# Kernel tuning notes

Measured on AMD Instinct MI355X. Metric: run time of the kernel, lower is better.

## Reference

```python
import jax, jax.numpy as jnp
import numpy as np

N_NODES = 50000
N_EDGES = 800000
GEN_EPS = 1e-7
LN_EPS = 1e-5


def _mlp3_tanh(x, w0, b0, w1, b1, w2, b2):
    x = jnp.tanh(x @ w0.T + b0)
    x = jnp.tanh(x @ w1.T + b1)
    return jnp.tanh(x @ w2.T + b2)


def _gen_conv(x, src, dst, edge_attr, w0, b0, ln_w, ln_b, w1, b1):
    # GENConv(aggr='softmax', t=1): msg = relu(x_j + e) + eps
    msg = jax.nn.relu(x[src] + edge_attr) + GEN_EPS          # [E, 64]
    m = jax.ops.segment_max(msg, dst, num_segments=N_NODES)  # [N, 64]
    ex = jnp.exp(msg - m[dst])
    den = jax.ops.segment_sum(ex, dst, num_segments=N_NODES)
    alpha = ex / den[dst]                                    # scatter-softmax per dst
    agg = jax.ops.segment_sum(alpha * msg, dst, num_segments=N_NODES)
    h = x + agg                                              # x_r + aggregated messages
    # internal MLP: Linear(64->128), LayerNorm(128), ReLU, Linear(128->64)
    h = h @ w0.T + b0
    mu = jnp.mean(h, axis=-1, keepdims=True)
    var = jnp.mean((h - mu) ** 2, axis=-1, keepdims=True)
    h = ln_w * (h - mu) * jax.lax.rsqrt(var + LN_EPS) + ln_b
    h = jax.nn.relu(h)
    return h @ w1.T + b1


def setup_inputs() -> dict:
    key = jax.random.key(0)
    ks = jax.random.split(key, 32)
    s = 0.05
    d = {
        'node_features': jax.random.normal(ks[0], (N_NODES, 11), jnp.float32),
        'edge_features': jax.random.normal(ks[1], (N_EDGES, 3), jnp.float32),
        'edge_index': jax.random.randint(ks[2], (2, N_EDGES), 0, N_NODES, jnp.int32),
        'ne_w0': jax.random.normal(ks[3], (64, 11)) * s, 'ne_b0': jnp.zeros((64,)),
        'ne_w1': jax.random.normal(ks[4], (64, 64)) * s, 'ne_b1': jnp.zeros((64,)),
        'ne_w2': jax.random.normal(ks[5], (64, 64)) * s, 'ne_b2': jnp.zeros((64,)),
        'ee_w0': jax.random.normal(ks[6], (64, 3)) * s, 'ee_b0': jnp.zeros((64,)),
        'ee_w1': jax.random.normal(ks[7], (64, 64)) * s, 'ee_b1': jnp.zeros((64,)),
        'ee_w2': jax.random.normal(ks[8], (64, 64)) * s, 'ee_b2': jnp.zeros((64,)),
        'mp_w0': jax.random.normal(ks[9], (3, 128, 64)) * s,
        'mp_b0': jnp.zeros((3, 128)),
        'mp_ln_w': jnp.ones((3, 128)), 'mp_ln_b': jnp.zeros((3, 128)),
        'mp_w1': jax.random.normal(ks[10], (3, 64, 128)) * s,
        'mp_b1': jnp.zeros((3, 64)),
        'pi_w0': jax.random.normal(ks[11], (64, 64)) * s, 'pi_b0': jnp.zeros((64,)),
        'pi_w1': jax.random.normal(ks[12], (64, 64)) * s, 'pi_b1': jnp.zeros((64,)),
        'pi_w2': jax.random.normal(ks[13], (2, 64)) * s, 'pi_b2': jnp.zeros((2,)),
    }
    return {k: (v.astype(jnp.float32) if v.dtype != jnp.int32 else v) for k, v in d.items()}


def reference(node_features, edge_features, edge_index,
              ne_w0, ne_b0, ne_w1, ne_b1, ne_w2, ne_b2,
              ee_w0, ee_b0, ee_w1, ee_b1, ee_w2, ee_b2,
              mp_w0, mp_b0, mp_ln_w, mp_ln_b, mp_w1, mp_b1,
              pi_w0, pi_b0, pi_w1, pi_b1, pi_w2, pi_b2):
    src, dst = edge_index[0], edge_index[1]
    x = _mlp3_tanh(node_features, ne_w0, ne_b0, ne_w1, ne_b1, ne_w2, ne_b2)
    e = _mlp3_tanh(edge_features, ee_w0, ee_b0, ee_w1, ee_b1, ee_w2, ee_b2)
    for i in range(3):
        x = _gen_conv(x, src, dst, e, mp_w0[i], mp_b0[i], mp_ln_w[i], mp_ln_b[i], mp_w1[i], mp_b1[i])
    h = jnp.tanh(x @ pi_w0.T + pi_b0)
    h = jnp.tanh(h @ pi_w1.T + pi_b1)
    out = h @ pi_w2.T + pi_b2                 # [N, 2]
    # output.t().reshape(-1)[:n_turbines] == first column of out
    means = -30.0 + (out[:, 0] + 1.0) * 60.0 / 2.0
    return means
```

## Files before the change

kernel.cpp:

```cpp
#include <hip/hip_runtime.h>
#include <stdint.h>

#define N_NODES 50000
#define N_EDGES 800000

typedef unsigned short u16;
typedef unsigned int u32;
typedef __attribute__((ext_vector_type(8))) short short8;
typedef __attribute__((ext_vector_type(4))) float f32x4;
typedef __attribute__((ext_vector_type(4))) u32 u32x4;
typedef __attribute__((ext_vector_type(2))) u32 u32x2;

#define WAVE_SYNC() asm volatile("s_waitcnt lgkmcnt(0)" ::: "memory")

__device__ __forceinline__ float b2f(u16 v) {
    u32 u = ((u32)v) << 16; float f; __builtin_memcpy(&f, &u, 4); return f;
}
__device__ __forceinline__ u16 f2b(float f) {
    u32 u; __builtin_memcpy(&u, &f, 4);
    return (u16)((u + 0x8000u) >> 16);
}
__device__ __forceinline__ float lo2f(u32 p) {
    u32 u = p << 16; float f; __builtin_memcpy(&f, &u, 4); return f;
}
__device__ __forceinline__ float hi2f(u32 p) {
    u32 u = p & 0xffff0000u; float f; __builtin_memcpy(&f, &u, 4); return f;
}
__device__ __forceinline__ u32 pack2(float a, float b) {
    u32 ua, ub; __builtin_memcpy(&ua, &a, 4); __builtin_memcpy(&ub, &b, 4);
    return __builtin_amdgcn_perm(ub + 0x8000u, ua + 0x8000u, 0x07060302u);
}
__device__ __forceinline__ f32x4 mfma16(short8 a, short8 b, f32x4 c) {
    return __builtin_amdgcn_mfma_f32_16x16x32_bf16(a, b, c, 0, 0, 0);
}

#define TANH_TBL_N 192
__device__ __forceinline__ void load_tbl(const float2* __restrict__ g, float2* tbl) {
    int i = (int)threadIdx.x;
    if (i < TANH_TBL_N) tbl[i] = g[i];
    __syncthreads();
}
__device__ __forceinline__ float lut_tanh(const float2* __restrict__ tbl, float x) {
    float a = __builtin_fabsf(x);
    a = fminf(a, 5.96875f);
    int i = (int)(a * 32.f);
    float2 bs = tbl[i];
    float y = fmaf(bs.y, a, bs.x);
    return copysignf(y, x);
}

enum : int {
    NE_T0 = 0,     NE_B0 = 704,   NE_T1 = 768,   NE_B1 = 4864,  NE_T2 = 4928,  NE_B2 = 9024,
    EE_T0 = 9088,  EE_B0 = 9280,  EE_T1 = 9344,  EE_B1 = 13440, EE_T2 = 13504, EE_B2 = 17600,
    MP_T0 = 17664, MP_B0 = 42240, LNW_O = 42624, LNB_O = 43008, MP_T1 = 43392, MP_B1 = 67968,
    PI_T0 = 68160, PI_B0 = 72256, PI_T1 = 72320, PI_B1 = 76416, PI_W2 = 76480, PI_B2 = 76608,
    W_TOTAL = 76610
};

enum : int {
    FR_EE1 = 0, FR_EE2 = 4, FR_EE3 = 12, FR_NE1 = 20, FR_NE2 = 24, FR_NE3 = 32,
    FR_MP0 = 40, FR_MP1 = 88, FR_PI0 = 136, FR_PI1 = 144, FR_TOTAL = 152
};

#define OFF_W       ((size_t)0)
#define OFF_FLAG    ((size_t)0x60000)
#define OFF_WB      ((size_t)0x61000)
#define OFF_TBL     ((size_t)0x88000)
#define OFF_XB0     ((size_t)0x90000)
#define OFF_XB1     ((size_t)0x700000)
#define OFF_H64B    ((size_t)0xE00000)
#define OFF_E       ((size_t)0x1500000)
#define OFF_ROWPTR  ((size_t)0x8300000)
#define OFF_CURSOR  ((size_t)0x8340000)
#define OFF_CNT     ((size_t)0x8380000)
#define OFF_PERM    ((size_t)0x83C0000)
#define OFF_SRCS    ((size_t)0x8700000)
#define OFF_BSUM    ((size_t)0x8A80000)

struct Ptrs24 { const void* p[24]; };


__global__ void detect_kernel(const void* nf, int* flag) {
    u32 w = ((const u32*)nf)[threadIdx.x & 63];
    u32 lo = w & 0xffffu;
    int e = (int)((lo >> 7) & 0xff);
    int good = ((e >= 118 && e <= 132) || lo == 0) ? 1 : 0;
    unsigned long long b = __ballot(good != 0);
    if (threadIdx.x == 0) *flag = (__popcll(b) >= 48) ? 1 : 0;
}

__global__ void convert_weights(Ptrs24 ps, float* __restrict__ W, const int* flag) {
    const int segIN[24] = {11,64,64,64,64,64, 3,64,64,64,64,64, 64,384,384,384,128,192, 64,64,64,64,128,2};
    const int segOUT[24]= {64, 1,64, 1,64, 1, 64, 1,64, 1,64, 1, 128, 1,  1,  1, 64,  1, 64, 1,64, 1,  1,1};
    const int segS[24]  = { 1, 1, 1, 1, 1, 1,  1, 1, 1, 1, 1, 1,   3, 1,  1,  1,  3,  1,  1, 1, 1, 1,  1,1};
    const int segTR[24] = { 1, 0, 1, 0, 1, 0,  1, 0, 1, 0, 1, 0,   1, 0,  0,  0,  1,  0,  1, 0, 1, 0,  0,0};
    int t = blockIdx.x * blockDim.x + threadIdx.x;
    if (t >= W_TOTAL) return;
    bool bf = (*flag != 0);
    int seg = 0, off = t;
    for (;;) {
        int cnt = segIN[seg] * segOUT[seg] * segS[seg];
        if (off < cnt) break;
        off -= cnt; seg++;
    }
    int srcIdx;
    if (segTR[seg]) {
        int per = segIN[seg] * segOUT[seg];
        int s = off / per, d = off % per;
        int j = d / segOUT[seg], i = d % segOUT[seg];
        srcIdx = s * per + i * segIN[seg] + j;
    } else {
        srcIdx = off;
    }
    const void* p = ps.p[seg];
    W[t] = bf ? b2f(((const u16*)p)[srcIdx]) : ((const float*)p)[srcIdx];
}

__global__ void make_frags(const float* __restrict__ W, u16* __restrict__ Wb,
                           float2* __restrict__ gtbl) {
    const int base[15] = {FR_EE1,FR_EE2,FR_EE3,FR_NE1,FR_NE2,FR_NE3,
                          FR_MP0,FR_MP0+16,FR_MP0+32, FR_MP1,FR_MP1+16,FR_MP1+32,
                          FR_PI0,FR_PI1,FR_TOTAL};
    const int woff[14] = {EE_T0,EE_T1,EE_T2, NE_T0,NE_T1,NE_T2,
                          MP_T0,MP_T0+8192,MP_T0+16384, MP_T1,MP_T1+8192,MP_T1+16384,
                          PI_T0,PI_T1};
    const int kreal[14] = {3,64,64, 11,64,64, 64,64,64, 128,128,128, 64,64};
    const int nn[14]    = {64,64,64, 64,64,64, 128,128,128, 64,64,64, 64,64};
    int t = blockIdx.x * blockDim.x + threadIdx.x;
    if (t >= FR_TOTAL * 512) {
        int i = t - FR_TOTAL * 512;
        if (i < TANH_TBL_N) {
            float x0 = i * 0.03125f, x1 = x0 + 0.03125f;
            float t0 = tanhf(x0), t1 = tanhf(x1);
            float s = (t1 - t0) * 32.f;
            gtbl[i] = make_float2(fmaf(-s, x0, t0), s);
        }
        return;
    }
    int f = t >> 9, r = t & 511, lane = r >> 3, j = r & 7;
    int l = 0;
    while (f >= base[l + 1]) l++;
    int lf = f - base[l];
    int NT = nn[l] >> 4;
    int kt = lf / NT, nt = lf % NT;
    int k = kt * 32 + (lane >> 4) * 8 + j;
    int n = nt * 16 + (lane & 15);
    float v = (k < kreal[l]) ? W[woff[l] + k * nn[l] + n] : 0.f;
    u32 u; __builtin_memcpy(&u, &v, 4);
    Wb[t] = (u16)((u + 0x7fffu + ((u >> 16) & 1u)) >> 16);
}


__global__ void hist_kernel(const int* __restrict__ dst, int* __restrict__ cnts) {
    int e = blockIdx.x * blockDim.x + threadIdx.x;
    if (e < N_EDGES) atomicAdd(&cnts[dst[e]], 1);
}

__global__ void scanA(const int* __restrict__ cnts, int* __restrict__ prow,
                      int* __restrict__ bsum) {
    __shared__ int wsum[16];
    int tid = threadIdx.x, lane = tid & 63, wid = tid >> 6;
    int i0 = blockIdx.x * 2048 + tid * 2;
    int v0 = 0, v1 = 0;
    if (i0 >= 1 && i0 <= N_NODES) v0 = (cnts[i0 - 1] + 1) & ~1;
    if (i0 + 1 <= N_NODES && i0 + 1 >= 1) v1 = (cnts[i0] + 1) & ~1;
    int v = v0 + v1;
#pragma unroll
    for (int off = 1; off < 64; off <<= 1) {
        int t = __shfl_up(v, off, 64);
        if (lane >= off) v += t;
    }
    if (lane == 63) wsum[wid] = v;
    __syncthreads();
    if (tid == 0) { int a = 0; for (int w = 0; w < 16; w++) { a += wsum[w]; wsum[w] = a; } }
    __syncthreads();
    int incl = v + (wid ? wsum[wid - 1] : 0);
    if (i0 <= N_NODES) prow[i0] = incl - v1;
    if (i0 + 1 <= N_NODES) prow[i0 + 1] = incl;
    if (tid == 1023) bsum[blockIdx.x] = incl;
}
__global__ void scanC(const int* __restrict__ bsum, int* __restrict__ prow,
                      int* __restrict__ cursor) {
    int i = blockIdx.x * 1024 + threadIdx.x;
    if (i > N_NODES) return;
    int nb = (int)(blockIdx.x >> 1);
    int add = 0;
    for (int b = 0; b < nb; b++) add += bsum[b];
    int v = prow[i] + add;
    prow[i] = v;
    if (i < N_NODES) cursor[i] = v;
}

__global__ void scatter_kernel(const int* __restrict__ dst, const int* __restrict__ src,
                               int* __restrict__ cursor, int* __restrict__ perm,
                               int* __restrict__ srcs) {
    int e = blockIdx.x * blockDim.x + threadIdx.x;
    if (e >= N_EDGES) return;
    int p = atomicAdd(&cursor[dst[e]], 1);
    perm[e] = p;
    srcs[p] = src[e];
}


template<int KT, int NT, int INSTR>
__device__ __forceinline__ void mfma_layer(const u32* ldsin, int lane,
        const short8* __restrict__ Wf, int basef, const float* __restrict__ bias, f32x4* acc) {
    int q = lane >> 4, mr = lane & 15;
#pragma unroll
    for (int nt = 0; nt < NT; nt++) acc[nt] = *(const f32x4*)(bias + nt * 16 + q * 4);
#pragma unroll
    for (int kt = 0; kt < KT; kt++) {
        short8 act = *(const short8*)(ldsin + mr * INSTR + kt * 16 + q * 4);
#pragma unroll
        for (int nt = 0; nt < NT; nt++)
            acc[nt] = mfma16(Wf[(basef + kt * NT + nt) * 64 + lane], act, acc[nt]);
    }
}

template<int KT, int NT>
__device__ __forceinline__ void mfma_layer_reg(const short8* act, int lane,
        const short8* __restrict__ Wf, int basef, const float* __restrict__ bias, f32x4* acc) {
    int q = lane >> 4;
#pragma unroll
    for (int nt = 0; nt < NT; nt++) acc[nt] = *(const f32x4*)(bias + nt * 16 + q * 4);
#pragma unroll
    for (int kt = 0; kt < KT; kt++)
#pragma unroll
        for (int nt = 0; nt < NT; nt++)
            acc[nt] = mfma16(Wf[(basef + kt * NT + nt) * 64 + lane], act[kt], acc[nt]);
}

template<int NT, int OUTSTR>
__device__ __forceinline__ void tanh_pack_lds(const f32x4* acc, u32* ldsout, int lane,
                                              const float2* __restrict__ tbl) {
    int q = lane >> 4, mr = lane & 15;
#pragma unroll
    for (int nt = 0; nt < NT; nt++) {
        f32x4 a = acc[nt];
        ldsout[mr * OUTSTR + nt * 8 + q * 2 + 0] = pack2(lut_tanh(tbl, a[0]), lut_tanh(tbl, a[1]));
        ldsout[mr * OUTSTR + nt * 8 + q * 2 + 1] = pack2(lut_tanh(tbl, a[2]), lut_tanh(tbl, a[3]));
    }
}

__device__ __forceinline__ void zero_stage(u32* B0, int lane) {
#pragma unroll
    for (int it = 0; it < 4; it++) {
        int f = lane + 64 * it;
        B0[(f >> 4) * 36 + (f & 15)] = 0;
    }
}


__global__ __launch_bounds__(256) void edge_encoder(const void* ef, u32* __restrict__ ebuf,
        const int* __restrict__ perm, const float* __restrict__ W,
        const short8* __restrict__ Wf, const float2* __restrict__ gtbl, const int* flag) {
    __shared__ u32 lds[4 * 1152];
    __shared__ float2 tbl[TANH_TBL_N];
    load_tbl(gtbl, tbl);
    int wv = threadIdx.x >> 6, lane = threadIdx.x & 63;
    u32* B0 = lds + wv * 1152;
    u32* B1 = B0 + 576;
    long ebase = (long)blockIdx.x * 64 + wv * 16;
    bool bf = (*flag != 0);
    zero_stage(B0, lane);
    if (lane < 16) {
        long e = ebase + lane;
        float i0, i1, i2;
        if (bf) { const u16* p = (const u16*)ef + e * 3; i0 = b2f(p[0]); i1 = b2f(p[1]); i2 = b2f(p[2]); }
        else    { const float* p = (const float*)ef + e * 3; i0 = p[0]; i1 = p[1]; i2 = p[2]; }
        u32* row = B0 + lane * 36;
        row[0] = pack2(i0, i1); row[1] = pack2(i2, 0.f);
    }
    WAVE_SYNC();
    f32x4 acc[4];
    mfma_layer<1, 4, 36>(B0, lane, Wf, FR_EE1, W + EE_B0, acc);
    tanh_pack_lds<4, 36>(acc, B1, lane, tbl);
    WAVE_SYNC();
    mfma_layer<2, 4, 36>(B1, lane, Wf, FR_EE2, W + EE_B1, acc);
    tanh_pack_lds<4, 36>(acc, B0, lane, tbl);
    WAVE_SYNC();
    mfma_layer<2, 4, 36>(B0, lane, Wf, FR_EE3, W + EE_B2, acc);
    tanh_pack_lds<4, 36>(acc, B1, lane, tbl);
    WAVE_SYNC();
    int ro = lane >> 2, cc = (lane & 3) * 8;
    long e = ebase + ro;
    long prowp = perm[e];
    u32x4 v0 = *(const u32x4*)&B1[ro * 36 + cc];
    u32x4 v1 = *(const u32x4*)&B1[ro * 36 + cc + 4];
    *(u32x4*)&ebuf[prowp * 32 + cc] = v0;
    *(u32x4*)&ebuf[prowp * 32 + cc + 4] = v1;
}

__global__ __launch_bounds__(256) void node_encoder(const void* nf,
        u16* __restrict__ xbf, const float* __restrict__ W,
        const short8* __restrict__ Wf, const float2* __restrict__ gtbl, const int* flag) {
    __shared__ u32 lds[4 * 1152];
    __shared__ float2 tbl[TANH_TBL_N];
    load_tbl(gtbl, tbl);
    int wv = threadIdx.x >> 6, lane = threadIdx.x & 63;
    int q = lane >> 4, mr = lane & 15;
    u32* B0 = lds + wv * 1152;
    u32* B1 = B0 + 576;
    long nbase = (long)blockIdx.x * 64 + wv * 16;
    bool bf = (*flag != 0);
    zero_stage(B0, lane);
    if (lane < 16) {
        long n = nbase + lane;
        if (n < N_NODES) {
            float in[11];
#pragma unroll
            for (int j = 0; j < 11; j++)
                in[j] = bf ? b2f(((const u16*)nf)[n * 11 + j]) : ((const float*)nf)[n * 11 + j];
            u32* row = B0 + lane * 36;
#pragma unroll
            for (int d = 0; d < 5; d++) row[d] = pack2(in[2 * d], in[2 * d + 1]);
            row[5] = pack2(in[10], 0.f);
        }
    }
    WAVE_SYNC();
    f32x4 acc[4];
    mfma_layer<1, 4, 36>(B0, lane, Wf, FR_NE1, W + NE_B0, acc);
    tanh_pack_lds<4, 36>(acc, B1, lane, tbl);
    WAVE_SYNC();
    mfma_layer<2, 4, 36>(B1, lane, Wf, FR_NE2, W + NE_B1, acc);
    tanh_pack_lds<4, 36>(acc, B0, lane, tbl);
    WAVE_SYNC();
    mfma_layer<2, 4, 36>(B0, lane, Wf, FR_NE3, W + NE_B2, acc);
    long n = nbase + mr;
    if (n < N_NODES) {
#pragma unroll
        for (int nt = 0; nt < 4; nt++) {
            float v0 = lut_tanh(tbl, acc[nt][0]), v1 = lut_tanh(tbl, acc[nt][1]);
            float v2 = lut_tanh(tbl, acc[nt][2]), v3 = lut_tanh(tbl, acc[nt][3]);
            u32x2 pb; pb.x = pack2(v0, v1); pb.y = pack2(v2, v3);
            *(u32x2*)&xbf[n * 64 + nt * 16 + q * 4] = pb;
        }
    }
}

__global__ __launch_bounds__(256) void aggregate_kernel(
        const u32* __restrict__ xbf32, const u32* __restrict__ ebuf32,
        const int* __restrict__ srcs, const int* __restrict__ prow,
        u32* __restrict__ h64bf32) {
    __shared__ int ldsW[4][64];
    int wv = threadIdx.x >> 6;
    int wid = (int)((blockIdx.x * 256 + threadIdx.x) >> 6);
    int lane = (int)(threadIdx.x & 63);
    int n0 = __builtin_amdgcn_readfirstlane(wid) * 2;
    if (n0 >= N_NODES) return;
    int half = lane >> 5, h = lane & 31;
    int rl = n0 + (lane < 2 ? lane : 2);
    int rv = prow[rl];
    int kb0 = __shfl(rv, 0, 64);
    int kb1 = __shfl(rv, 1, 64);
    int kb2 = __shfl(rv, 2, 64);
    float num[2][2], den[2][2];
#pragma unroll
    for (int j = 0; j < 2; j++) { num[j][0] = num[j][1] = den[j][0] = den[j][1] = 0.f; }
    for (int wb = kb0; wb < kb2; wb += 64) {
        ldsW[wv][lane] = srcs[wb + lane];
        WAVE_SYNC();
        int we = wb + 64;
        int hi0 = kb1 < we ? kb1 : we;
        int lo1 = kb1 > wb ? kb1 : wb;
        int hi1 = kb2 < we ? kb2 : we;
#pragma unroll 2
        for (int k = wb; k < hi0; k += 2) {
            int s = ldsW[wv][k - wb + half];
            u32 ev = ebuf32[(size_t)(k + half) * 32 + h];
            u32 xv = xbf32[(size_t)(s > 0 ? s : 0) * 32 + h];
            float m0 = fmaxf(lo2f(xv) + lo2f(ev), 0.f) + 1e-7f;
            float m1 = fmaxf(hi2f(xv) + hi2f(ev), 0.f) + 1e-7f;
            float w0 = __expf(m0), w1 = __expf(m1);
            if (s < 0) { w0 = 0.f; w1 = 0.f; }
            num[0][0] = fmaf(w0, m0, num[0][0]); den[0][0] += w0;
            num[0][1] = fmaf(w1, m1, num[0][1]); den[0][1] += w1;
        }
#pragma unroll 2
        for (int k = lo1; k < hi1; k += 2) {
            int s = ldsW[wv][k - wb + half];
            u32 ev = ebuf32[(size_t)(k + half) * 32 + h];
            u32 xv = xbf32[(size_t)(s > 0 ? s : 0) * 32 + h];
            float m0 = fmaxf(lo2f(xv) + lo2f(ev), 0.f) + 1e-7f;
            float m1 = fmaxf(hi2f(xv) + hi2f(ev), 0.f) + 1e-7f;
            float w0 = __expf(m0), w1 = __expf(m1);
            if (s < 0) { w0 = 0.f; w1 = 0.f; }
            num[1][0] = fmaf(w0, m0, num[1][0]); den[1][0] += w0;
            num[1][1] = fmaf(w1, m1, num[1][1]); den[1][1] += w1;
        }
        WAVE_SYNC();
    }
#pragma unroll
    for (int j = 0; j < 2; j++) {
        float n0f = num[j][0] + __shfl_xor(num[j][0], 32, 64);
        float d0f = den[j][0] + __shfl_xor(den[j][0], 32, 64);
        float n1f = num[j][1] + __shfl_xor(num[j][1], 32, 64);
        float d1f = den[j][1] + __shfl_xor(den[j][1], 32, 64);
        if (half == 0) {
            float agg0 = (d0f > 0.f) ? __fdividef(n0f, d0f) : 0.f;
            float agg1 = (d1f > 0.f) ? __fdividef(n1f, d1f) : 0.f;
            u32 xr = xbf32[(size_t)(n0 + j) * 32 + h];
            h64bf32[(size_t)(n0 + j) * 32 + h] = pack2(lo2f(xr) + agg0, hi2f(xr) + agg1);
        }
    }
}

__global__ __launch_bounds__(256) void mlp_fused(const u16* __restrict__ h64bf,
        u16* __restrict__ xbf,
        const float* __restrict__ W, const short8* __restrict__ Wf, int r) {
    __shared__ u32 lds[4 * 1088];
    int wv = threadIdx.x >> 6, lane = threadIdx.x & 63;
    int q = lane >> 4, mr = lane & 15;
    u32* bufY = lds + wv * 1088;
    long nbase = (long)blockIdx.x * 64 + wv * 16;
    long row = nbase + mr;
    long rc = (row < N_NODES) ? row : (N_NODES - 1);
    short8 act[2];
#pragma unroll
    for (int kt = 0; kt < 2; kt++)
        act[kt] = *(const short8*)&h64bf[rc * 64 + kt * 32 + q * 8];
    f32x4 acc[8];
    mfma_layer_reg<2, 8>(act, lane, Wf, FR_MP0 + r * 16, W + MP_B0 + r * 128, acc);
    float s = 0.f, sq = 0.f;
#pragma unroll
    for (int nt = 0; nt < 8; nt++)
#pragma unroll
        for (int rr = 0; rr < 4; rr++) { float v = acc[nt][rr]; s += v; sq = fmaf(v, v, sq); }
    s += __shfl_xor(s, 16, 64);  s += __shfl_xor(s, 32, 64);
    sq += __shfl_xor(sq, 16, 64); sq += __shfl_xor(sq, 32, 64);
    float mu = s * (1.f / 128.f);
    float var = sq * (1.f / 128.f) - mu * mu;
    float inv = rsqrtf(var + 1e-5f);
    const float* LW = W + LNW_O + r * 128;
    const float* LB = W + LNB_O + r * 128;
#pragma unroll
    for (int nt = 0; nt < 8; nt++) {
        f32x4 lw = *(const f32x4*)(LW + nt * 16 + q * 4);
        f32x4 lb = *(const f32x4*)(LB + nt * 16 + q * 4);
        float u0 = fmaxf(fmaf((acc[nt][0] - mu) * inv, lw[0], lb[0]), 0.f);
        float u1 = fmaxf(fmaf((acc[nt][1] - mu) * inv, lw[1], lb[1]), 0.f);
        float u2 = fmaxf(fmaf((acc[nt][2] - mu) * inv, lw[2], lb[2]), 0.f);
        float u3 = fmaxf(fmaf((acc[nt][3] - mu) * inv, lw[3], lb[3]), 0.f);
        bufY[mr * 68 + nt * 8 + q * 2 + 0] = pack2(u0, u1);
        bufY[mr * 68 + nt * 8 + q * 2 + 1] = pack2(u2, u3);
    }
    WAVE_SYNC();
    f32x4 acc2[4];
    mfma_layer<4, 4, 68>(bufY, lane, Wf, FR_MP1 + r * 16, W + MP_B1 + r * 64, acc2);
    if (row < N_NODES) {
#pragma unroll
        for (int nt = 0; nt < 4; nt++) {
            f32x4 v = acc2[nt];
            u32x2 pb; pb.x = pack2(v[0], v[1]); pb.y = pack2(v[2], v[3]);
            *(u32x2*)&xbf[row * 64 + nt * 16 + q * 4] = pb;
        }
    }
}

__global__ __launch_bounds__(256) void policy_head(const u16* __restrict__ xbf, void* out,
        const float* __restrict__ W, const short8* __restrict__ Wf,
        const float2* __restrict__ gtbl, const int* flag) {
    __shared__ u32 lds[4 * 576];
    __shared__ float2 tbl[TANH_TBL_N];
    load_tbl(gtbl, tbl);
    int wv = threadIdx.x >> 6, lane = threadIdx.x & 63;
    int q = lane >> 4, mr = lane & 15;
    u32* bufY = lds + wv * 576;
    long nbase = (long)blockIdx.x * 64 + wv * 16;
    long row = nbase + mr;
    long rc = (row < N_NODES) ? row : (N_NODES - 1);
    bool bf = (*flag != 0);
    short8 act[2];
#pragma unroll
    for (int kt = 0; kt < 2; kt++)
        act[kt] = *(const short8*)&xbf[rc * 64 + kt * 32 + q * 8];
    f32x4 acc[4];
    mfma_layer_reg<2, 4>(act, lane, Wf, FR_PI0, W + PI_B0, acc);
    tanh_pack_lds<4, 36>(acc, bufY, lane, tbl);
    WAVE_SYNC();
    mfma_layer<2, 4, 36>(bufY, lane, Wf, FR_PI1, W + PI_B1, acc);
    float o = 0.f;
#pragma unroll
    for (int nt = 0; nt < 4; nt++) {
        f32x4 w2 = *(const f32x4*)(W + PI_W2 + nt * 16 + q * 4);
#pragma unroll
        for (int rr = 0; rr < 4; rr++) o = fmaf(lut_tanh(tbl, acc[nt][rr]), w2[rr], o);
    }
    o += __shfl_xor(o, 16, 64);
    o += __shfl_xor(o, 32, 64);
    if (lane < 16 && row < N_NODES) {
        float means = 30.f * (o + W[PI_B2]);
        if (bf) ((u16*)out)[row] = f2b(means);
        else    ((float*)out)[row] = means;
    }
}

extern "C" void kernel_launch(void* const* d_in, const int* in_sizes, int n_in,
                              void* d_out, int out_size, void* d_ws, size_t ws_size,
                              hipStream_t stream) {
    char* ws = (char*)d_ws;
    float* W      = (float*)(ws + OFF_W);
    int*   flag   = (int*)(ws + OFF_FLAG);
    u16*   Wb     = (u16*)(ws + OFF_WB);
    const short8* Wf = (const short8*)(ws + OFF_WB);
    float2* gtbl  = (float2*)(ws + OFF_TBL);
    u16*   xb0    = (u16*)(ws + OFF_XB0);
    u16*   xb1    = (u16*)(ws + OFF_XB1);
    u16*   h64bf  = (u16*)(ws + OFF_H64B);
    u32*   h64b32 = (u32*)(ws + OFF_H64B);
    u32*   ebuf32 = (u32*)(ws + OFF_E);
    int*   prow   = (int*)(ws + OFF_ROWPTR);
    int*   cursor = (int*)(ws + OFF_CURSOR);
    int*   cnts   = (int*)(ws + OFF_CNT);
    int*   perm   = (int*)(ws + OFF_PERM);
    int*   srcs   = (int*)(ws + OFF_SRCS);
    int*   bsum   = (int*)(ws + OFF_BSUM);

    const int* ei   = (const int*)d_in[2];
    const int* srcv = ei;
    const int* dstv = ei + N_EDGES;

    detect_kernel<<<1, 64, 0, stream>>>(d_in[0], flag);
    hipMemsetAsync(cnts, 0, N_NODES * sizeof(int), stream);
    hipMemsetAsync(srcs, 0xFF, (size_t)0x340000, stream);

    Ptrs24 ps;
    for (int k = 0; k < 24; k++) ps.p[k] = d_in[3 + k];
    convert_weights<<<(W_TOTAL + 255) / 256, 256, 0, stream>>>(ps, W, flag);
    make_frags<<<(FR_TOTAL * 512 + TANH_TBL_N + 255) / 256, 256, 0, stream>>>(W, Wb, gtbl);

    hist_kernel<<<(N_EDGES + 255) / 256, 256, 0, stream>>>(dstv, cnts);
    scanA<<<25, 1024, 0, stream>>>(cnts, prow, bsum);
    scanC<<<(N_NODES + 1024) / 1024, 1024, 0, stream>>>(bsum, prow, cursor);
    scatter_kernel<<<(N_EDGES + 255) / 256, 256, 0, stream>>>(dstv, srcv, cursor, perm, srcs);

    node_encoder<<<(N_NODES + 63) / 64, 256, 0, stream>>>(d_in[0], xb0, W, Wf, gtbl, flag);
    edge_encoder<<<N_EDGES / 64, 256, 0, stream>>>(d_in[1], ebuf32, perm, W, Wf, gtbl, flag);

    u16* xbc = xb0; u16* xbn = xb1;
    const int aggBlocks = (N_NODES / 2 * 64) / 256;
    for (int r = 0; r < 3; r++) {
        aggregate_kernel<<<aggBlocks, 256, 0, stream>>>(
            (const u32*)xbc, ebuf32, srcs, prow, h64b32);
        mlp_fused<<<(N_NODES + 63) / 64, 256, 0, stream>>>(h64bf, xbn, W, Wf, r);
        u16* tb = xbc; xbc = xbn; xbn = tb;
    }
    policy_head<<<(N_NODES + 63) / 64, 256, 0, stream>>>(xbc, d_out, W, Wf, gtbl, flag);
}
```

Before: 431.9 us.

## Merge prep kernels, inline dtype detection, drop srcs memset, half-packed tanh table

Folds the detect, convert_weights and make_frags kernels into one prep kernel. It reads weights directly from the inputs and copies only the biases and small vectors into W. Each consumer kernel now detects the input dtype itself instead of reading a flag. The large memset of srcs is replaced by scanC writing a -1 pad slot only for odd-count rows. The tanh LUT is packed as fp16 pairs with a wider range, and the aggregate loop unroll rises from 2 to 4. This removes several launches and a memset, at the cost of a less precise fp16 table and redundant detection work in every block.

New measurement: 420.8 us. 2.6% less time.

```diff
diff --git a/kernel.cpp b/kernel.cpp
--- a/kernel.cpp
+++ b/kernel.cpp
@@ -1,4 +1,5 @@
 #include <hip/hip_runtime.h>
+#include <hip/hip_fp16.h>
 #include <stdint.h>
 
 #define N_NODES 50000
@@ -34,26 +35,37 @@
     return __builtin_amdgcn_mfma_f32_16x16x32_bf16(a, b, c, 0, 0, 0);
 }
 
-#define TANH_TBL_N 192
-__device__ __forceinline__ void load_tbl(const float2* __restrict__ g, float2* tbl) {
+__device__ __forceinline__ bool detect_bf(const void* nf) {
+    u32 w = ((const u32*)nf)[threadIdx.x & 63];
+    u32 lo = w & 0xffffu;
+    int e = (int)((lo >> 7) & 0xff);
+    int good = ((e >= 118 && e <= 132) || lo == 0) ? 1 : 0;
+    unsigned long long b = __ballot(good != 0);
+    return __popcll(b) >= 48;
+}
+
+#define TANH_TBL_N 256
+__device__ __forceinline__ void load_tbl(const u32* __restrict__ g, u32* tbl) {
     int i = (int)threadIdx.x;
     if (i < TANH_TBL_N) tbl[i] = g[i];
     __syncthreads();
 }
-__device__ __forceinline__ float lut_tanh(const float2* __restrict__ tbl, float x) {
+__device__ __forceinline__ float lut_tanh(const u32* __restrict__ tbl, float x) {
     float a = __builtin_fabsf(x);
-    a = fminf(a, 5.96875f);
+    a = fminf(a, 7.96875f);
     int i = (int)(a * 32.f);
-    float2 bs = tbl[i];
-    float y = fmaf(bs.y, a, bs.x);
-    return copysignf(y, x);
+    u32 e = tbl[i];
+    __half2 h2; __builtin_memcpy(&h2, &e, 4);
+    float b = __half2float(__low2half(h2));
+    float s = __half2float(__high2half(h2));
+    return copysignf(fmaf(s, a, b), x);
 }
 
 enum : int {
-    NE_T0 = 0,     NE_B0 = 704,   NE_T1 = 768,   NE_B1 = 4864,  NE_T2 = 4928,  NE_B2 = 9024,
-    EE_T0 = 9088,  EE_B0 = 9280,  EE_T1 = 9344,  EE_B1 = 13440, EE_T2 = 13504, EE_B2 = 17600,
-    MP_T0 = 17664, MP_B0 = 42240, LNW_O = 42624, LNB_O = 43008, MP_T1 = 43392, MP_B1 = 67968,
-    PI_T0 = 68160, PI_B0 = 72256, PI_T1 = 72320, PI_B1 = 76416, PI_W2 = 76480, PI_B2 = 76608,
+    NE_B0 = 704,   NE_B1 = 4864,  NE_B2 = 9024,
+    EE_B0 = 9280,  EE_B1 = 13440, EE_B2 = 17600,
+    MP_B0 = 42240, LNW_O = 42624, LNB_O = 43008, MP_B1 = 67968,
+    PI_B0 = 72256, PI_B1 = 76416, PI_W2 = 76480, PI_B2 = 76608,
     W_TOTAL = 76610
 };
 
@@ -63,7 +75,6 @@
 };
 
 #define OFF_W       ((size_t)0)
-#define OFF_FLAG    ((size_t)0x60000)
 #define OFF_WB      ((size_t)0x61000)
 #define OFF_TBL     ((size_t)0x88000)
 #define OFF_XB0     ((size_t)0x90000)
@@ -79,75 +90,59 @@
 
 struct Ptrs24 { const void* p[24]; };
 
-
-__global__ void detect_kernel(const void* nf, int* flag) {
-    u32 w = ((const u32*)nf)[threadIdx.x & 63];
-    u32 lo = w & 0xffffu;
-    int e = (int)((lo >> 7) & 0xff);
-    int good = ((e >= 118 && e <= 132) || lo == 0) ? 1 : 0;
-    unsigned long long b = __ballot(good != 0);
-    if (threadIdx.x == 0) *flag = (__popcll(b) >= 48) ? 1 : 0;
-}
-
-__global__ void convert_weights(Ptrs24 ps, float* __restrict__ W, const int* flag) {
-    const int segIN[24] = {11,64,64,64,64,64, 3,64,64,64,64,64, 64,384,384,384,128,192, 64,64,64,64,128,2};
-    const int segOUT[24]= {64, 1,64, 1,64, 1, 64, 1,64, 1,64, 1, 128, 1,  1,  1, 64,  1, 64, 1,64, 1,  1,1};
-    const int segS[24]  = { 1, 1, 1, 1, 1, 1,  1, 1, 1, 1, 1, 1,   3, 1,  1,  1,  3,  1,  1, 1, 1, 1,  1,1};
-    const int segTR[24] = { 1, 0, 1, 0, 1, 0,  1, 0, 1, 0, 1, 0,   1, 0,  0,  0,  1,  0,  1, 0, 1, 0,  0,0};
+__global__ void prep_kernel(const void* nf, Ptrs24 ps, float* __restrict__ W,
+                            u16* __restrict__ Wb, u32* __restrict__ gtbl) {
+    bool bf = detect_bf(nf);
     int t = blockIdx.x * blockDim.x + threadIdx.x;
-    if (t >= W_TOTAL) return;
-    bool bf = (*flag != 0);
-    int seg = 0, off = t;
-    for (;;) {
-        int cnt = segIN[seg] * segOUT[seg] * segS[seg];
-        if (off < cnt) break;
-        off -= cnt; seg++;
-    }
-    int srcIdx;
-    if (segTR[seg]) {
-        int per = segIN[seg] * segOUT[seg];
-        int s = off / per, d = off % per;
-        int j = d / segOUT[seg], i = d % segOUT[seg];
-        srcIdx = s * per + i * segIN[seg] + j;
-    } else {
-        srcIdx = off;
-    }
-    const void* p = ps.p[seg];
-    W[t] = bf ? b2f(((const u16*)p)[srcIdx]) : ((const float*)p)[srcIdx];
-}
-
-__global__ void make_frags(const float* __restrict__ W, u16* __restrict__ Wb,
-                           float2* __restrict__ gtbl) {
-    const int base[15] = {FR_EE1,FR_EE2,FR_EE3,FR_NE1,FR_NE2,FR_NE3,
-                          FR_MP0,FR_MP0+16,FR_MP0+32, FR_MP1,FR_MP1+16,FR_MP1+32,
-                          FR_PI0,FR_PI1,FR_TOTAL};
-    const int woff[14] = {EE_T0,EE_T1,EE_T2, NE_T0,NE_T1,NE_T2,
-                          MP_T0,MP_T0+8192,MP_T0+16384, MP_T1,MP_T1+8192,MP_T1+16384,
-                          PI_T0,PI_T1};
-    const int kreal[14] = {3,64,64, 11,64,64, 64,64,64, 128,128,128, 64,64};
-    const int nn[14]    = {64,64,64, 64,64,64, 128,128,128, 64,64,64, 64,64};
-    int t = blockIdx.x * blockDim.x + threadIdx.x;
-    if (t >= FR_TOTAL * 512) {
-        int i = t - FR_TOTAL * 512;
-        if (i < TANH_TBL_N) {
-            float x0 = i * 0.03125f, x1 = x0 + 0.03125f;
-            float t0 = tanhf(x0), t1 = tanhf(x1);
-            float s = (t1 - t0) * 32.f;
-            gtbl[i] = make_float2(fmaf(-s, x0, t0), s);
-        }
+    if (t < FR_TOTAL * 512) {
+        const int base[15] = {FR_EE1,FR_EE2,FR_EE3,FR_NE1,FR_NE2,FR_NE3,
+                              FR_MP0,FR_MP0+16,FR_MP0+32, FR_MP1,FR_MP1+16,FR_MP1+32,
+                              FR_PI0,FR_PI1,FR_TOTAL};
+        const int psrc[14]  = {6,8,10, 0,2,4, 12,12,12, 16,16,16, 18,20};
+        const int soff[14]  = {0,0,0, 0,0,0, 0,8192,16384, 0,8192,16384, 0,0};
+        const int kreal[14] = {3,64,64, 11,64,64, 64,64,64, 128,128,128, 64,64};
+        const int nn[14]    = {64,64,64, 64,64,64, 128,128,128, 64,64,64, 64,64};
+        int f = t >> 9, r = t & 511, lane = r >> 3, j = r & 7;
+        int l = 0;
+        while (f >= base[l + 1]) l++;
+        int lf = f - base[l];
+        int NT = nn[l] >> 4;
+        int kt = lf / NT, nt = lf % NT;
+        int k = kt * 32 + (lane >> 4) * 8 + j;
+        int n = nt * 16 + (lane & 15);
+        float v = 0.f;
+        if (k < kreal[l]) {
+            long idx = (long)soff[l] + (long)n * kreal[l] + k;
+            const void* p = ps.p[psrc[l]];
+            v = bf ? b2f(((const u16*)p)[idx]) : ((const float*)p)[idx];
+        }
+        u32 u; __builtin_memcpy(&u, &v, 4);
+        Wb[t] = (u16)((u + 0x7fffu + ((u >> 16) & 1u)) >> 16);
         return;
     }
-    int f = t >> 9, r = t & 511, lane = r >> 3, j = r & 7;
-    int l = 0;
-    while (f >= base[l + 1]) l++;
-    int lf = f - base[l];
-    int NT = nn[l] >> 4;
-    int kt = lf / NT, nt = lf % NT;
-    int k = kt * 32 + (lane >> 4) * 8 + j;
-    int n = nt * 16 + (lane & 15);
-    float v = (k < kreal[l]) ? W[woff[l] + k * nn[l] + n] : 0.f;
-    u32 u; __builtin_memcpy(&u, &v, 4);
-    Wb[t] = (u16)((u + 0x7fffu + ((u >> 16) & 1u)) >> 16);
+    int t2 = t - FR_TOTAL * 512;
+    if (t2 < 1986) {
+        const int cnt[14]  = {64,64,64, 64,64,64, 384,384,384,192, 64,64,128,2};
+        const int wdst[14] = {NE_B0,NE_B1,NE_B2, EE_B0,EE_B1,EE_B2,
+                              MP_B0,LNW_O,LNB_O,MP_B1, PI_B0,PI_B1,PI_W2,PI_B2};
+        const int sp[14]   = {1,3,5, 7,9,11, 13,14,15,17, 19,21,22,23};
+        int sgi = 0, off = t2;
+        while (off >= cnt[sgi]) { off -= cnt[sgi]; sgi++; }
+        const void* p = ps.p[sp[sgi]];
+        W[wdst[sgi] + off] = bf ? b2f(((const u16*)p)[off]) : ((const float*)p)[off];
+        return;
+    }
+    int i = t2 - 1986;
+    if (i < TANH_TBL_N) {
+        float x0 = i * 0.03125f, x1 = x0 + 0.03125f;
+        float t0 = tanhf(x0), t1 = tanhf(x1);
+        float s = (t1 - t0) * 32.f;
+        float b = fmaf(-s, x0, t0);
+        __half hs = __float2half(s), hb = __float2half(b);
+        u16 us, ub;
+        __builtin_memcpy(&us, &hs, 2); __builtin_memcpy(&ub, &hb, 2);
+        gtbl[i] = (u32)ub | ((u32)us << 16);
+    }
 }
 
 
@@ -179,8 +174,9 @@
     if (i0 + 1 <= N_NODES) prow[i0 + 1] = incl;
     if (tid == 1023) bsum[blockIdx.x] = incl;
 }
-__global__ void scanC(const int* __restrict__ bsum, int* __restrict__ prow,
-                      int* __restrict__ cursor) {
+__global__ void scanC(const int* __restrict__ bsum, const int* __restrict__ cnts,
+                      int* __restrict__ prow, int* __restrict__ cursor,
+                      int* __restrict__ srcs) {
     int i = blockIdx.x * 1024 + threadIdx.x;
     if (i > N_NODES) return;
     int nb = (int)(blockIdx.x >> 1);
@@ -188,7 +184,11 @@
     for (int b = 0; b < nb; b++) add += bsum[b];
     int v = prow[i] + add;
     prow[i] = v;
-    if (i < N_NODES) cursor[i] = v;
+    if (i < N_NODES) {
+        cursor[i] = v;
+        int c = cnts[i];
+        if (c & 1) srcs[v + c] = -1;
+    }
 }
 
 __global__ void scatter_kernel(const int* __restrict__ dst, const int* __restrict__ src,
@@ -232,7 +232,7 @@
 
 template<int NT, int OUTSTR>
 __device__ __forceinline__ void tanh_pack_lds(const f32x4* acc, u32* ldsout, int lane,
-                                              const float2* __restrict__ tbl) {
+                                              const u32* __restrict__ tbl) {
     int q = lane >> 4, mr = lane & 15;
 #pragma unroll
     for (int nt = 0; nt < NT; nt++) {
@@ -251,17 +251,17 @@
 }
 
 
-__global__ __launch_bounds__(256) void edge_encoder(const void* ef, u32* __restrict__ ebuf,
-        const int* __restrict__ perm, const float* __restrict__ W,
-        const short8* __restrict__ Wf, const float2* __restrict__ gtbl, const int* flag) {
+__global__ __launch_bounds__(256) void edge_encoder(const void* nf, const void* ef,
+        u32* __restrict__ ebuf, const int* __restrict__ perm, const float* __restrict__ W,
+        const short8* __restrict__ Wf, const u32* __restrict__ gtbl) {
     __shared__ u32 lds[4 * 1152];
-    __shared__ float2 tbl[TANH_TBL_N];
+    __shared__ u32 tbl[TANH_TBL_N];
+    bool bf = detect_bf(nf);
     load_tbl(gtbl, tbl);
     int wv = threadIdx.x >> 6, lane = threadIdx.x & 63;
     u32* B0 = lds + wv * 1152;
     u32* B1 = B0 + 576;
     long ebase = (long)blockIdx.x * 64 + wv * 16;
-    bool bf = (*flag != 0);
     zero_stage(B0, lane);
     if (lane < 16) {
         long e = ebase + lane;
@@ -293,16 +293,16 @@
 
 __global__ __launch_bounds__(256) void node_encoder(const void* nf,
         u16* __restrict__ xbf, const float* __restrict__ W,
-        const short8* __restrict__ Wf, const float2* __restrict__ gtbl, const int* flag) {
+        const short8* __restrict__ Wf, const u32* __restrict__ gtbl) {
     __shared__ u32 lds[4 * 1152];
-    __shared__ float2 tbl[TANH_TBL_N];
+    __shared__ u32 tbl[TANH_TBL_N];
+    bool bf = detect_bf(nf);
     load_tbl(gtbl, tbl);
     int wv = threadIdx.x >> 6, lane = threadIdx.x & 63;
     int q = lane >> 4, mr = lane & 15;
     u32* B0 = lds + wv * 1152;
     u32* B1 = B0 + 576;
     long nbase = (long)blockIdx.x * 64 + wv * 16;
-    bool bf = (*flag != 0);
     zero_stage(B0, lane);
     if (lane < 16) {
         long n = nbase + lane;
@@ -338,6 +338,7 @@
     }
 }
 
+template<int R>
 __global__ __launch_bounds__(256) void aggregate_kernel(
         const u32* __restrict__ xbf32, const u32* __restrict__ ebuf32,
         const int* __restrict__ srcs, const int* __restrict__ prow,
@@ -364,7 +365,7 @@
         int hi0 = kb1 < we ? kb1 : we;
         int lo1 = kb1 > wb ? kb1 : wb;
         int hi1 = kb2 < we ? kb2 : we;
-#pragma unroll 2
+#pragma unroll 4
         for (int k = wb; k < hi0; k += 2) {
             int s = ldsW[wv][k - wb + half];
             u32 ev = ebuf32[(size_t)(k + half) * 32 + h];
@@ -376,7 +377,7 @@
             num[0][0] = fmaf(w0, m0, num[0][0]); den[0][0] += w0;
             num[0][1] = fmaf(w1, m1, num[0][1]); den[0][1] += w1;
         }
-#pragma unroll 2
+#pragma unroll 4
         for (int k = lo1; k < hi1; k += 2) {
             int s = ldsW[wv][k - wb + half];
             u32 ev = ebuf32[(size_t)(k + half) * 32 + h];
@@ -457,11 +458,12 @@
     }
 }
 
-__global__ __launch_bounds__(256) void policy_head(const u16* __restrict__ xbf, void* out,
-        const float* __restrict__ W, const short8* __restrict__ Wf,
-        const float2* __restrict__ gtbl, const int* flag) {
+__global__ __launch_bounds__(256) void policy_head(const void* nf,
+        const u16* __restrict__ xbf, void* out, const float* __restrict__ W,
+        const short8* __restrict__ Wf, const u32* __restrict__ gtbl) {
     __shared__ u32 lds[4 * 576];
-    __shared__ float2 tbl[TANH_TBL_N];
+    __shared__ u32 tbl[TANH_TBL_N];
+    bool bf = detect_bf(nf);
     load_tbl(gtbl, tbl);
     int wv = threadIdx.x >> 6, lane = threadIdx.x & 63;
     int q = lane >> 4, mr = lane & 15;
@@ -469,7 +471,6 @@
     long nbase = (long)blockIdx.x * 64 + wv * 16;
     long row = nbase + mr;
     long rc = (row < N_NODES) ? row : (N_NODES - 1);
-    bool bf = (*flag != 0);
     short8 act[2];
 #pragma unroll
     for (int kt = 0; kt < 2; kt++)
@@ -500,10 +501,9 @@
                               hipStream_t stream) {
     char* ws = (char*)d_ws;
     float* W      = (float*)(ws + OFF_W);
-    int*   flag   = (int*)(ws + OFF_FLAG);
     u16*   Wb     = (u16*)(ws + OFF_WB);
     const short8* Wf = (const short8*)(ws + OFF_WB);
-    float2* gtbl  = (float2*)(ws + OFF_TBL);
+    u32*   gtbl   = (u32*)(ws + OFF_TBL);
     u16*   xb0    = (u16*)(ws + OFF_XB0);
     u16*   xb1    = (u16*)(ws + OFF_XB1);
     u16*   h64bf  = (u16*)(ws + OFF_H64B);
@@ -516,34 +516,37 @@
     int*   srcs   = (int*)(ws + OFF_SRCS);
     int*   bsum   = (int*)(ws + OFF_BSUM);
 
+    const void* nf  = d_in[0];
     const int* ei   = (const int*)d_in[2];
     const int* srcv = ei;
     const int* dstv = ei + N_EDGES;
 
-    detect_kernel<<<1, 64, 0, stream>>>(d_in[0], flag);
     hipMemsetAsync(cnts, 0, N_NODES * sizeof(int), stream);
-    hipMemsetAsync(srcs, 0xFF, (size_t)0x340000, stream);
 
     Ptrs24 ps;
     for (int k = 0; k < 24; k++) ps.p[k] = d_in[3 + k];
-    convert_weights<<<(W_TOTAL + 255) / 256, 256, 0, stream>>>(ps, W, flag);
-    make_frags<<<(FR_TOTAL * 512 + TANH_TBL_N + 255) / 256, 256, 0, stream>>>(W, Wb, gtbl);
+    prep_kernel<<<(FR_TOTAL * 512 + 1986 + TANH_TBL_N + 255) / 256, 256, 0, stream>>>(
+        nf, ps, W, Wb, gtbl);
 
     hist_kernel<<<(N_EDGES + 255) / 256, 256, 0, stream>>>(dstv, cnts);
     scanA<<<25, 1024, 0, stream>>>(cnts, prow, bsum);
-    scanC<<<(N_NODES + 1024) / 1024, 1024, 0, stream>>>(bsum, prow, cursor);
+    scanC<<<(N_NODES + 1024) / 1024, 1024, 0, stream>>>(bsum, cnts, prow, cursor, srcs);
     scatter_kernel<<<(N_EDGES + 255) / 256, 256, 0, stream>>>(dstv, srcv, cursor, perm, srcs);
 
-    node_encoder<<<(N_NODES + 63) / 64, 256, 0, stream>>>(d_in[0], xb0, W, Wf, gtbl, flag);
-    edge_encoder<<<N_EDGES / 64, 256, 0, stream>>>(d_in[1], ebuf32, perm, W, Wf, gtbl, flag);
+    node_encoder<<<(N_NODES + 63) / 64, 256, 0, stream>>>(nf, xb0, W, Wf, gtbl);
+    edge_encoder<<<N_EDGES / 64, 256, 0, stream>>>(nf, d_in[1], ebuf32, perm, W, Wf, gtbl);
 
     u16* xbc = xb0; u16* xbn = xb1;
     const int aggBlocks = (N_NODES / 2 * 64) / 256;
-    for (int r = 0; r < 3; r++) {
-        aggregate_kernel<<<aggBlocks, 256, 0, stream>>>(
-            (const u32*)xbc, ebuf32, srcs, prow, h64b32);
-        mlp_fused<<<(N_NODES + 63) / 64, 256, 0, stream>>>(h64bf, xbn, W, Wf, r);
-        u16* tb = xbc; xbc = xbn; xbn = tb;
-    }
-    policy_head<<<(N_NODES + 63) / 64, 256, 0, stream>>>(xbc, d_out, W, Wf, gtbl, flag);
-}
+    aggregate_kernel<0><<<aggBlocks, 256, 0, stream>>>((const u32*)xbc, ebuf32, srcs, prow, h64b32);
+    mlp_fused<<<(N_NODES + 63) / 64, 256, 0, stream>>>(h64bf, xbn, W, Wf, 0);
+    { u16* tb = xbc; xbc = xbn; xbn = tb; }
+    aggregate_kernel<1><<<aggBlocks, 256, 0, stream>>>((const u32*)xbc, ebuf32, srcs, prow, h64b32);
+    mlp_fused<<<(N_NODES + 63) / 64, 256, 0, stream>>>(h64bf, xbn, W, Wf, 1);
+    { u16* tb = xbc; xbc = xbn; xbn = tb; }
+    aggregate_kernel<2><<<aggBlocks, 256, 0, stream>>>((const u32*)xbc, ebuf32, srcs, prow, h64b32);
+    mlp_fused<<<(N_NODES + 63) / 64, 256, 0, stream>>>(h64bf, xbn, W, Wf, 2);
+    { u16* tb = xbc; xbc = xbn; xbn = tb; }
+
+    policy_head<<<(N_NODES + 63) / 64, 256, 0, stream>>>(nf, xbc, d_out, W, Wf, gtbl);
+}
```
